# Kernel tuning notes

Hardware: AMD Instinct MI355X
Metric: run time of the kernel (lower is better)

## Reference

```python
import jax, jax.numpy as jnp
import numpy as np

HEADS = 16
DIM_HEAD = 64
DIM = 1024
EPS = 1e-12  # F.normalize eps


def setup_inputs() -> dict:
    key = jax.random.key(0)
    ks = jax.random.split(key, 8)
    b, n = 2, 2048
    dim_inner = HEADS * DIM_HEAD
    return {
        "x": jax.random.normal(ks[0], (b, n, DIM), dtype=jnp.float32),
        "value_residual": jax.random.normal(ks[1], (b, HEADS, n, DIM_HEAD), dtype=jnp.float32),
        "gamma": jnp.ones((DIM,), dtype=jnp.float32),
        "w_qkv": jax.random.normal(ks[2], (DIM, dim_inner * 3), dtype=jnp.float32) * 0.02,
        "w_mix": jax.random.normal(ks[3], (DIM, HEADS), dtype=jnp.float32) * 0.02,
        "b_mix": jnp.zeros((HEADS,), dtype=jnp.float32),
        "w_gates": jax.random.normal(ks[4], (DIM, HEADS), dtype=jnp.float32) * 0.02,
        "b_gates": jnp.zeros((HEADS,), dtype=jnp.float32),
        "w_out": jax.random.normal(ks[5], (dim_inner, DIM), dtype=jnp.float32) * 0.02,
    }


def reference(x, value_residual, gamma, w_qkv, w_mix, b_mix, w_gates, b_gates, w_out):
    b, n, dim = x.shape
    scale = DIM_HEAD ** -0.5

    # RMSNorm: F.normalize(x, dim=-1) * sqrt(dim) * gamma
    l2 = jnp.maximum(jnp.linalg.norm(x, axis=-1, keepdims=True), EPS)
    xn = x / l2 * (dim ** 0.5) * gamma

    # QKV projection, split to [b, h, n, d]
    qkv = xn @ w_qkv                                  # [b, n, 3*h*d]
    qkv = qkv.reshape(b, n, 3, HEADS, DIM_HEAD)
    q, k, v = [jnp.transpose(qkv[:, :, i], (0, 2, 1, 3)) for i in range(3)]
    orig_v = v

    # value-residual lerp: v.lerp(value_residual, mix) = v + mix*(vr - v)
    mix = jax.nn.sigmoid(xn @ w_mix + b_mix)          # [b, n, h]
    mix = jnp.transpose(mix, (0, 2, 1))[..., None]    # [b, h, n, 1]
    v = v + mix * (value_residual - v)

    # scaled dot-product attention
    scores = jnp.einsum('bhnd,bhmd->bhnm', q, k) * scale
    attn = jax.nn.softmax(scores, axis=-1)
    out = jnp.einsum('bhnm,bhmd->bhnd', attn, v)      # [b, h, n, d]

    # sigmoid gating per head
    gates = jax.nn.sigmoid(xn @ w_gates + b_gates)    # [b, n, h]
    gates = jnp.transpose(gates, (0, 2, 1))[..., None]
    out = out * gates

    out = jnp.transpose(out, (0, 2, 1, 3)).reshape(b, n, HEADS * DIM_HEAD)
    return out @ w_out, orig_v
```

## Files before the change

### kernel.cpp

```cpp
#include <hip/hip_runtime.h>
#include <math.h>

#define HEADS 16
#define DHEAD 64
#define DIMM 1024
#define NQKV 3072
#define NB 2
#define SEQ 2048
#define MROWS 4096

typedef unsigned short ushort_t;
typedef unsigned int uint_t;
typedef __attribute__((ext_vector_type(8))) short short8;
typedef __attribute__((ext_vector_type(8))) unsigned short u16x8;
typedef __attribute__((ext_vector_type(16))) float f32x16;

__device__ __forceinline__ ushort_t f2bf(float f) {
  uint_t u = __float_as_uint(f);
  u += 0x7fffu + ((u >> 16) & 1u);
  return (ushort_t)(u >> 16);
}

__device__ __forceinline__ uint_t cvtpk_bf16(float lo, float hi) {
  uint_t r;
  asm("v_cvt_pk_bf16_f32 %0, %1, %2" : "=v"(r) : "v"(lo), "v"(hi));
  return r;
}

__device__ __forceinline__ f32x16 mfma32(short8 a, short8 b, f32x16 c) {
  return __builtin_amdgcn_mfma_f32_32x32x16_bf16(a, b, c, 0, 0, 0);
}

__device__ __forceinline__ void gload_lds16(const void* g, void* l) {
  __builtin_amdgcn_global_load_lds(
      (const __attribute__((address_space(1))) void*)g,
      (__attribute__((address_space(3))) void*)l, 16, 0, 0);
}

__global__ __launch_bounds__(256) void k_rmsnorm(const float* __restrict__ x,
                                                 const float* __restrict__ gamma,
                                                 ushort_t* __restrict__ xn_bf) {
  int row = blockIdx.x;
  int t = threadIdx.x;
  float4 v = reinterpret_cast<const float4*>(x + (size_t)row * DIMM)[t];
  float ss = v.x * v.x + v.y * v.y + v.z * v.z + v.w * v.w;
#pragma unroll
  for (int o = 32; o >= 1; o >>= 1) ss += __shfl_xor(ss, o, 64);
  __shared__ float red[4];
  if ((t & 63) == 0) red[t >> 6] = ss;
  __syncthreads();
  ss = red[0] + red[1] + red[2] + red[3];
  float s = 32.0f / fmaxf(sqrtf(ss), 1e-12f);
  float4 g = reinterpret_cast<const float4*>(gamma)[t];
  ushort4 ob;
  ob.x = f2bf(v.x * s * g.x);
  ob.y = f2bf(v.y * s * g.y);
  ob.z = f2bf(v.z * s * g.z);
  ob.w = f2bf(v.w * s * g.w);
  *reinterpret_cast<ushort4*>(xn_bf + (size_t)row * DIMM + t * 4) = ob;
}

__global__ __launch_bounds__(256) void k_pack_w(const float* __restrict__ w_mix,
                                                const float* __restrict__ w_gates,
                                                ushort_t* __restrict__ wt) {
  int o = blockIdx.x;
  const float* w = (o < HEADS) ? (w_mix + o) : (w_gates + (o - HEADS));
  for (int k = threadIdx.x; k < DIMM; k += 256)
    wt[(size_t)o * DIMM + k] = f2bf(w[(size_t)k * HEADS]);
}

__global__ __launch_bounds__(64) void k_mixgates_mfma(const ushort_t* __restrict__ xn_bf,
                                                      const ushort_t* __restrict__ wt,
                                                      const float* __restrict__ b_mix,
                                                      const float* __restrict__ b_gates,
                                                      float* __restrict__ mg) {
  const int l = threadIdx.x;
  const int ln = l & 31;
  const int hi = l >> 5;
  const int m0 = blockIdx.x * 32;
  const uint4* arow = reinterpret_cast<const uint4*>(xn_bf + (size_t)(m0 + ln) * DIMM);
  const uint4* brow = reinterpret_cast<const uint4*>(wt + (size_t)ln * DIMM);
  f32x16 acc;
#pragma unroll
  for (int r = 0; r < 16; ++r) acc[r] = 0.f;
#pragma unroll 8
  for (int ks = 0; ks < 64; ++ks) {
    uint4 ta = arow[ks * 2 + hi];
    uint4 tb = brow[ks * 2 + hi];
    acc = mfma32(*reinterpret_cast<short8*>(&ta), *reinterpret_cast<short8*>(&tb), acc);
  }
  float bias = (ln < HEADS) ? b_mix[ln] : b_gates[ln - HEADS];
#pragma unroll
  for (int r = 0; r < 16; ++r) {
    int row = m0 + (r & 3) + 8 * (r >> 2) + 4 * hi;
    float val = acc[r] + bias;
    mg[(size_t)row * 32 + ln] = 1.f / (1.f + __expf(-val));
  }
}

__global__ __launch_bounds__(256) void k_transpose_bf(const float* __restrict__ in,
                                                      ushort_t* __restrict__ outT,
                                                      int N, int K) {
  __shared__ float tile[32][33];
  int n0 = blockIdx.x * 32, k0 = blockIdx.y * 32;
  int t = threadIdx.x;
  int r = t >> 3, c4 = (t & 7) * 4;
  float4 v = *reinterpret_cast<const float4*>(in + (size_t)(k0 + r) * N + n0 + c4);
  tile[r][c4 + 0] = v.x; tile[r][c4 + 1] = v.y; tile[r][c4 + 2] = v.z; tile[r][c4 + 3] = v.w;
  __syncthreads();
  ushort4 o;
  o.x = f2bf(tile[c4 + 0][r]);
  o.y = f2bf(tile[c4 + 1][r]);
  o.z = f2bf(tile[c4 + 2][r]);
  o.w = f2bf(tile[c4 + 3][r]);
  *reinterpret_cast<ushort4*>(outT + (size_t)(n0 + r) * K + k0 + c4) = o;
}

template <int NCOLS, int MODE>
__global__ __launch_bounds__(256, 2) void k_gemm_bf(const ushort_t* __restrict__ A,
                                                    const ushort_t* __restrict__ Bt,
                                                    ushort_t* __restrict__ q_bf,
                                                    ushort_t* __restrict__ k_bf,
                                                    ushort_t* __restrict__ v_bf,
                                                    float* __restrict__ orig_v,
                                                    const float* __restrict__ vr,
                                                    const float* __restrict__ mg,
                                                    float* __restrict__ outp) {
  __shared__ __align__(16) ushort_t As[128 * 64];
  __shared__ __align__(16) ushort_t Bs[128 * 64];
  const int t = threadIdx.x;
  const int w = t >> 6;
  const int l = t & 63;
  const int ln = l & 31;
  const int hi = l >> 5;
  const int wm = w >> 1, wn = w & 1;
  const int m0 = blockIdx.y * 128, n0 = blockIdx.x * 128;

  f32x16 acc00, acc01, acc10, acc11;
#pragma unroll
  for (int r = 0; r < 16; ++r) { acc00[r] = 0.f; acc01[r] = 0.f; acc10[r] = 0.f; acc11[r] = 0.f; }

  const int srow8 = l >> 3;
  const int cp = l & 7;

  for (int k0 = 0; k0 < DIMM; k0 += 64) {
#pragma unroll
    for (int i = 0; i < 4; ++i) {
      int rowa = (i * 4 + w) * 8 + srow8;
      const ushort_t* ga = A + (size_t)(m0 + rowa) * DIMM + k0 + ((cp ^ (rowa & 7)) * 8);
      gload_lds16(ga, &As[(i * 4 + w) * 512]);
      const ushort_t* gb = Bt + (size_t)(n0 + rowa) * DIMM + k0 + ((cp ^ (rowa & 7)) * 8);
      gload_lds16(gb, &Bs[(i * 4 + w) * 512]);
    }
    __syncthreads();
#pragma unroll
    for (int ks = 0; ks < 4; ++ks) {
      int cl = ks * 2 + hi;
      int ra0 = wm * 64 + ln;
      int ra1 = wm * 64 + 32 + ln;
      int rb0 = wn * 64 + ln;
      int rb1 = wn * 64 + 32 + ln;
      short8 af0 = *reinterpret_cast<const short8*>(&As[ra0 * 64 + ((cl ^ (ra0 & 7)) * 8)]);
      short8 af1 = *reinterpret_cast<const short8*>(&As[ra1 * 64 + ((cl ^ (ra1 & 7)) * 8)]);
      short8 bf0 = *reinterpret_cast<const short8*>(&Bs[rb0 * 64 + ((cl ^ (rb0 & 7)) * 8)]);
      short8 bf1 = *reinterpret_cast<const short8*>(&Bs[rb1 * 64 + ((cl ^ (rb1 & 7)) * 8)]);
      acc00 = mfma32(af0, bf0, acc00);
      acc01 = mfma32(af0, bf1, acc01);
      acc10 = mfma32(af1, bf0, acc10);
      acc11 = mfma32(af1, bf1, acc11);
    }
    __syncthreads();
  }

  auto do_tile = [&](const f32x16& a, int mt, int nt) {
    int nb = n0 + wn * 64 + nt * 32;
    if (MODE == 1) {
#pragma unroll
      for (int r = 0; r < 16; ++r) {
        int m_loc = wm * 64 + mt * 32 + (r & 3) + 8 * (r >> 2) + 4 * hi;
        int row = m0 + m_loc;
        outp[(size_t)row * NCOLS + nb + ln] = a[r];
      }
    } else {
      int part = nb >> 10;
      int hh = (nb & 1023) >> 6;
      int ddb = (nb & 63) + ln;
#pragma unroll
      for (int r = 0; r < 16; ++r) {
        int m_loc = wm * 64 + mt * 32 + (r & 3) + 8 * (r >> 2) + 4 * hi;
        int row = m0 + m_loc;
        int b_i = row >> 11, n_i = row & 2047;
        size_t idx = (((size_t)(b_i * HEADS + hh)) * SEQ + n_i) * DHEAD + ddb;
        float val = a[r];
        if (part == 0) {
          q_bf[idx] = f2bf(val);
        } else if (part == 1) {
          k_bf[idx] = f2bf(val);
        } else {
          orig_v[idx] = val;
          float mixv = mg[(size_t)row * 32 + hh];
          float fv = val + mixv * (vr[idx] - val);
          v_bf[idx] = f2bf(fv);
        }
      }
    }
  };
  do_tile(acc00, 0, 0);
  do_tile(acc01, 0, 1);
  do_tile(acc10, 1, 0);
  do_tile(acc11, 1, 1);
}

__global__ __launch_bounds__(256, 2) void k_attn(const ushort_t* __restrict__ qb,
                                                 const ushort_t* __restrict__ kb,
                                                 const ushort_t* __restrict__ vb,
                                                 const float* __restrict__ mg,
                                                 ushort_t* __restrict__ attn_bf) {
  __shared__ uint4 Ksm[64 * 8];
  __shared__ uint_t Vtsm[64 * 32];

  const int t = threadIdx.x;
  const int w = t >> 6;
  const int l = t & 63;
  const int hi = l >> 5;
  const int ln = l & 31;
  const int bh = blockIdx.y;
  const int q0 = blockIdx.x * 128;
  const int b_i = bh >> 4, h = bh & 15;

  const size_t base = (size_t)bh * SEQ * DHEAD;

  short8 qf[4];
  {
    const uint4* qsrc = reinterpret_cast<const uint4*>(qb + base + (size_t)(q0 + w * 32 + ln) * DHEAD);
#pragma unroll
    for (int ds = 0; ds < 4; ++ds) {
      uint4 tq = qsrc[ds * 2 + hi];
      qf[ds] = *reinterpret_cast<short8*>(&tq);
    }
  }

  f32x16 o0, o1;
#pragma unroll
  for (int r = 0; r < 16; ++r) { o0[r] = 0.f; o1[r] = 0.f; }
  float m_run = -3.0e38f, l_run = 0.f;

  const int sr = t >> 2;
  const int sc = (t & 3) * 2;
  const int vp = t & 31;
  const int vg = t >> 5;

  const uint4* kg = reinterpret_cast<const uint4*>(kb + base);
  const uint4* vgp = reinterpret_cast<const uint4*>(vb + base);

  uint4 kA = kg[(size_t)sr * 8 + sc];
  uint4 kB = kg[(size_t)sr * 8 + sc + 1];
  uint4 vA = vgp[(size_t)(vp * 2) * 8 + vg];
  uint4 vB = vgp[(size_t)(vp * 2 + 1) * 8 + vg];

  for (int kt = 0; kt < SEQ / 64; ++kt) {
    __syncthreads();
    Ksm[sr * 8 + (sc ^ (sr & 7))] = kA;
    Ksm[sr * 8 + ((sc + 1) ^ (sr & 7))] = kB;
    {
      u16x8 a = *reinterpret_cast<u16x8*>(&vA);
      u16x8 b = *reinterpret_cast<u16x8*>(&vB);
#pragma unroll
      for (int j = 0; j < 8; ++j) {
        uint_t pw = (uint_t)a[j] | ((uint_t)b[j] << 16);
        int d = vg * 8 + j;
        Vtsm[d * 32 + (((vp >> 2) ^ j) << 2) + (vp & 3)] = pw;
      }
    }
    __syncthreads();

    if (kt + 1 < SEQ / 64) {
      size_t rb = (size_t)((kt + 1) * 64);
      kA = kg[(rb + sr) * 8 + sc];
      kB = kg[(rb + sr) * 8 + sc + 1];
      vA = vgp[(rb + vp * 2) * 8 + vg];
      vB = vgp[(rb + vp * 2 + 1) * 8 + vg];
    }

    f32x16 s0, s1;
#pragma unroll
    for (int r = 0; r < 16; ++r) { s0[r] = 0.f; s1[r] = 0.f; }
#pragma unroll
    for (int ds = 0; ds < 4; ++ds) {
      int ch = ds * 2 + hi;
      uint4 ta = Ksm[ln * 8 + (ch ^ (ln & 7))];
      s0 = mfma32(*reinterpret_cast<short8*>(&ta), qf[ds], s0);
      int r1 = 32 + ln;
      uint4 tb = Ksm[r1 * 8 + (ch ^ (r1 & 7))];
      s1 = mfma32(*reinterpret_cast<short8*>(&tb), qf[ds], s1);
    }

    float u[32];
#pragma unroll
    for (int r = 0; r < 16; ++r) { u[r] = s0[r]; u[16 + r] = s1[r]; }
    float mx = u[0];
#pragma unroll
    for (int r = 1; r < 32; ++r) mx = fmaxf(mx, u[r]);
    mx *= 0.125f;
    mx = fmaxf(mx, __shfl_xor(mx, 32, 64));
    float mnew = fmaxf(m_run, mx);
    float corr = __expf(m_run - mnew);
    m_run = mnew;
    float p[32];
    float rs = 0.f;
#pragma unroll
    for (int r = 0; r < 32; ++r) {
      p[r] = __expf(fmaf(u[r], 0.125f, -mnew));
      rs += p[r];
    }
    rs += __shfl_xor(rs, 32, 64);
    l_run = fmaf(l_run, corr, rs);
    o0 *= corr;
    o1 *= corr;

    short8 pa[4];
#pragma unroll
    for (int ks = 0; ks < 4; ++ks) {
      int g = ks * 8;
      uint_t w0 = cvtpk_bf16(p[g + 0], p[g + 1]);
      uint_t w1 = cvtpk_bf16(p[g + 2], p[g + 3]);
      uint_t w2 = cvtpk_bf16(p[g + 4], p[g + 5]);
      uint_t w3 = cvtpk_bf16(p[g + 6], p[g + 7]);
      asm volatile("v_permlane32_swap_b32 %0, %1" : "+v"(w0), "+v"(w2));
      asm volatile("v_permlane32_swap_b32 %0, %1" : "+v"(w1), "+v"(w3));
      uint_t tw[4] = {w0, w1, w2, w3};
      pa[ks] = *reinterpret_cast<short8*>(tw);
    }

#pragma unroll
    for (int ks = 0; ks < 4; ++ks) {
      int ch = ks * 2 + hi;
      uint4 ta = *reinterpret_cast<uint4*>(&Vtsm[ln * 32 + ((ch ^ (ln & 7)) << 2)]);
      o0 = mfma32(*reinterpret_cast<short8*>(&ta), pa[ks], o0);
      int d1 = 32 + ln;
      uint4 tb = *reinterpret_cast<uint4*>(&Vtsm[d1 * 32 + ((ch ^ (d1 & 7)) << 2)]);
      o1 = mfma32(*reinterpret_cast<short8*>(&tb), pa[ks], o1);
    }
  }

  int n_i = q0 + w * 32 + ln;
  int rowg = b_i * SEQ + n_i;
  float gate = mg[(size_t)rowg * 32 + HEADS + h];
  float f = gate / l_run;
  ushort_t* dst = attn_bf + (size_t)rowg * DIMM + h * DHEAD;
#pragma unroll
  for (int g = 0; g < 4; ++g) {
    uint2 p0;
    p0.x = cvtpk_bf16(o0[4 * g] * f, o0[4 * g + 1] * f);
    p0.y = cvtpk_bf16(o0[4 * g + 2] * f, o0[4 * g + 3] * f);
    *reinterpret_cast<uint2*>(dst + g * 8 + hi * 4) = p0;
    uint2 p1;
    p1.x = cvtpk_bf16(o1[4 * g] * f, o1[4 * g + 1] * f);
    p1.y = cvtpk_bf16(o1[4 * g + 2] * f, o1[4 * g + 3] * f);
    *reinterpret_cast<uint2*>(dst + 32 + g * 8 + hi * 4) = p1;
  }
}

extern "C" void kernel_launch(void* const* d_in, const int* in_sizes, int n_in,
                              void* d_out, int out_size, void* d_ws, size_t ws_size,
                              hipStream_t stream) {
  const float* x       = (const float*)d_in[0];
  const float* vr      = (const float*)d_in[1];
  const float* gamma   = (const float*)d_in[2];
  const float* w_qkv   = (const float*)d_in[3];
  const float* w_mix   = (const float*)d_in[4];
  const float* b_mix   = (const float*)d_in[5];
  const float* w_gates = (const float*)d_in[6];
  const float* b_gates = (const float*)d_in[7];
  const float* w_out   = (const float*)d_in[8];

  float* out = (float*)d_out;
  float* orig_v = out + (size_t)MROWS * DIMM;

  const size_t BUF = (size_t)MROWS * DIMM;
  char* wsb = (char*)d_ws;
  ushort_t* xn_bf   = (ushort_t*)wsb;                     wsb += BUF * 2;
  ushort_t* q_bf    = (ushort_t*)wsb;                     wsb += BUF * 2;
  ushort_t* k_bf    = (ushort_t*)wsb;                     wsb += BUF * 2;
  ushort_t* v_bf    = (ushort_t*)wsb;                     wsb += BUF * 2;
  ushort_t* attn_bf = (ushort_t*)wsb;                     wsb += BUF * 2;
  ushort_t* wqkv_t  = (ushort_t*)wsb;                     wsb += (size_t)NQKV * DIMM * 2;
  ushort_t* wout_t  = (ushort_t*)wsb;                     wsb += (size_t)DIMM * DIMM * 2;
  ushort_t* wt_mg   = (ushort_t*)wsb;                     wsb += (size_t)32 * DIMM * 2;
  float*    mg      = (float*)wsb;                        wsb += (size_t)MROWS * 32 * 4;

  k_pack_w<<<dim3(32), dim3(256), 0, stream>>>(w_mix, w_gates, wt_mg);
  k_transpose_bf<<<dim3(NQKV / 32, DIMM / 32), dim3(256), 0, stream>>>(w_qkv, wqkv_t, NQKV, DIMM);
  k_transpose_bf<<<dim3(DIMM / 32, DIMM / 32), dim3(256), 0, stream>>>(w_out, wout_t, DIMM, DIMM);
  k_rmsnorm<<<dim3(MROWS), dim3(256), 0, stream>>>(x, gamma, xn_bf);
  k_mixgates_mfma<<<dim3(MROWS / 32), dim3(64), 0, stream>>>(xn_bf, wt_mg, b_mix, b_gates, mg);
  k_gemm_bf<NQKV, 0><<<dim3(NQKV / 128, MROWS / 128), dim3(256), 0, stream>>>(
      xn_bf, wqkv_t, q_bf, k_bf, v_bf, orig_v, vr, mg, nullptr);
  k_attn<<<dim3(SEQ / 128, NB * HEADS), dim3(256), 0, stream>>>(q_bf, k_bf, v_bf, mg, attn_bf);
  k_gemm_bf<DIMM, 1><<<dim3(DIMM / 128, MROWS / 128), dim3(256), 0, stream>>>(
      attn_bf, wout_t, nullptr, nullptr, nullptr, nullptr, nullptr, nullptr, out);
}
```

Baseline: 250.2 us.

## Double-buffer GEMM LDS tiles and swizzle workgroup order

The bf16 MFMA GEMM now uses two LDS buffers, so the global-to-LDS loads for the next K tile are issued before the MFMAs on the current tile. This replaces the load-then-sync-then-compute pattern with one wait and barrier per iteration, aiming to hide memory latency. Workgroup indices are also remapped with a stride-8 swizzle to change which tiles run together and improve cache reuse. LDS use doubles to 64KB per block, which may limit occupancy under launch_bounds(256,2).

```diff
diff --git a/kernel.cpp b/kernel.cpp
--- a/kernel.cpp
+++ b/kernel.cpp
@@ -126,15 +126,20 @@
                                                     const float* __restrict__ vr,
                                                     const float* __restrict__ mg,
                                                     float* __restrict__ outp) {
-  __shared__ __align__(16) ushort_t As[128 * 64];
-  __shared__ __align__(16) ushort_t Bs[128 * 64];
+  __shared__ __align__(16) ushort_t As[2][128 * 64];
+  __shared__ __align__(16) ushort_t Bs[2][128 * 64];
   const int t = threadIdx.x;
   const int w = t >> 6;
   const int l = t & 63;
   const int ln = l & 31;
   const int hi = l >> 5;
   const int wm = w >> 1, wn = w & 1;
-  const int m0 = blockIdx.y * 128, n0 = blockIdx.x * 128;
+
+  constexpr int NBX = NCOLS / 128;
+  constexpr int NWG = NBX * (MROWS / 128);
+  int flat = blockIdx.y * NBX + blockIdx.x;
+  int swz = (flat & 7) * (NWG / 8) + (flat >> 3);
+  const int m0 = (swz / NBX) * 128, n0 = (swz % NBX) * 128;
 
   f32x16 acc00, acc01, acc10, acc11;
 #pragma unroll
@@ -143,16 +148,26 @@
   const int srow8 = l >> 3;
   const int cp = l & 7;
 
-  for (int k0 = 0; k0 < DIMM; k0 += 64) {
+  auto stage = [&](int buf, int k0) {
 #pragma unroll
     for (int i = 0; i < 4; ++i) {
       int rowa = (i * 4 + w) * 8 + srow8;
       const ushort_t* ga = A + (size_t)(m0 + rowa) * DIMM + k0 + ((cp ^ (rowa & 7)) * 8);
-      gload_lds16(ga, &As[(i * 4 + w) * 512]);
+      gload_lds16(ga, &As[buf][(i * 4 + w) * 512]);
       const ushort_t* gb = Bt + (size_t)(n0 + rowa) * DIMM + k0 + ((cp ^ (rowa & 7)) * 8);
-      gload_lds16(gb, &Bs[(i * 4 + w) * 512]);
-    }
-    __syncthreads();
+      gload_lds16(gb, &Bs[buf][(i * 4 + w) * 512]);
+    }
+  };
+
+  stage(0, 0);
+  asm volatile("s_waitcnt vmcnt(0)" ::: "memory");
+  __builtin_amdgcn_s_barrier();
+
+  for (int kt = 0; kt < DIMM / 64; ++kt) {
+    int cur = kt & 1;
+    if (kt + 1 < DIMM / 64) stage(cur ^ 1, (kt + 1) * 64);
+    const ushort_t* as = As[cur];
+    const ushort_t* bs = Bs[cur];
 #pragma unroll
     for (int ks = 0; ks < 4; ++ks) {
       int cl = ks * 2 + hi;
@@ -160,16 +175,17 @@
       int ra1 = wm * 64 + 32 + ln;
       int rb0 = wn * 64 + ln;
       int rb1 = wn * 64 + 32 + ln;
-      short8 af0 = *reinterpret_cast<const short8*>(&As[ra0 * 64 + ((cl ^ (ra0 & 7)) * 8)]);
-      short8 af1 = *reinterpret_cast<const short8*>(&As[ra1 * 64 + ((cl ^ (ra1 & 7)) * 8)]);
-      short8 bf0 = *reinterpret_cast<const short8*>(&Bs[rb0 * 64 + ((cl ^ (rb0 & 7)) * 8)]);
-      short8 bf1 = *reinterpret_cast<const short8*>(&Bs[rb1 * 64 + ((cl ^ (rb1 & 7)) * 8)]);
+      short8 af0 = *reinterpret_cast<const short8*>(&as[ra0 * 64 + ((cl ^ (ra0 & 7)) * 8)]);
+      short8 af1 = *reinterpret_cast<const short8*>(&as[ra1 * 64 + ((cl ^ (ra1 & 7)) * 8)]);
+      short8 bf0 = *reinterpret_cast<const short8*>(&bs[rb0 * 64 + ((cl ^ (rb0 & 7)) * 8)]);
+      short8 bf1 = *reinterpret_cast<const short8*>(&bs[rb1 * 64 + ((cl ^ (rb1 & 7)) * 8)]);
       acc00 = mfma32(af0, bf0, acc00);
       acc01 = mfma32(af0, bf1, acc01);
       acc10 = mfma32(af1, bf0, acc10);
       acc11 = mfma32(af1, bf1, acc11);
     }
-    __syncthreads();
+    asm volatile("s_waitcnt vmcnt(0)" ::: "memory");
+    __builtin_amdgcn_s_barrier();
   }
 
   auto do_tile = [&](const f32x16& a, int mt, int nt) {
```

After: 267.8 us. 1.07x slower.
